# Kernel optimization log

Measured on AMD Instinct MI355X. Metric: run time of the kernel, lower is better.

## Reference

```python
import jax, jax.numpy as jnp
import numpy as np

NUM_CLASSES = 256
MARGIN = 0.3
EPS = 1e-12  # torch F.normalize eps


def setup_inputs() -> dict:
    key = jax.random.key(0)
    k1, k2 = jax.random.split(key)
    embeddings = jax.random.normal(k1, (65536, 512), dtype=jnp.float32)
    labels = jax.random.randint(k2, (65536,), 0, NUM_CLASSES)
    return {"embeddings": embeddings, "labels": labels}


def _l2_normalize(x):
    n = jnp.linalg.norm(x, axis=-1, keepdims=True)
    return x / jnp.maximum(n, EPS)


def reference(embeddings, labels):
    # emb_norm: (B, d)
    emb = _l2_normalize(embeddings)

    # Per-class segment mean -> centroids (C, d)
    counts = jax.ops.segment_sum(jnp.ones((emb.shape[0],), emb.dtype), labels,
                                 num_segments=NUM_CLASSES)          # (C,)
    sums = jax.ops.segment_sum(emb, labels, num_segments=NUM_CLASSES)  # (C, d)
    present = counts > 0                                              # (C,)
    cent = sums / jnp.maximum(counts, 1.0)[:, None]
    cent = _l2_normalize(cent)

    # Pairwise centroid euclidean distances (centroids are unit-norm).
    # Only used for argmin (no grad path), so stop_gradient for safety.
    cg = jax.lax.stop_gradient(cent)
    dist = jnp.sqrt(jnp.clip(2.0 - 2.0 * (cg @ cg.T), 0.0))           # (C, C)
    inf = jnp.asarray(jnp.inf, dist.dtype)
    dist = jnp.where(jnp.eye(NUM_CLASSES, dtype=bool), inf, dist)
    dist = jnp.where(present[None, :], dist, inf)  # empty classes can't be negatives
    nearest = jnp.argmin(dist, axis=1)                                # (C,)

    # Gather positive / nearest-negative centroid per sample
    pos_c = cent[labels]                 # (B, d)
    neg_c = cent[nearest[labels]]        # (B, d)
    d_pos = 1.0 - jnp.sum(emb * pos_c, axis=1)
    d_neg = 1.0 - jnp.sum(emb * neg_c, axis=1)
    terms = jax.nn.relu(d_pos - d_neg + MARGIN)                       # (B,)

    # Per-class mean of triplet terms, then mean over present classes
    loss_c = jax.ops.segment_sum(terms, labels, num_segments=NUM_CLASSES)
    loss_c = loss_c / jnp.maximum(counts, 1.0)
    n_present = jnp.maximum(jnp.sum(present.astype(emb.dtype)), 1.0)
    loss = jnp.sum(jnp.where(present, loss_c, 0.0)) / n_present
    return loss
```

## Files before the change

### kernel.cpp

```cpp
#include <hip/hip_runtime.h>
#include <math.h>

#define BROWS 65536
#define DIMS 512
#define NCLS 256
#define MARGIN 0.3f
#define EPSN 1e-12f
#define TSPL 8
#define CURPAD 16

__global__ void __launch_bounds__(256) khist(const int* __restrict__ labels,
                                             float* __restrict__ counts) {
  __shared__ int h[NCLS];
  int t = threadIdx.x;
  h[t] = 0;
  __syncthreads();
  int base = blockIdx.x * 2048 + t;
#pragma unroll
  for (int k = 0; k < 8; ++k) atomicAdd(&h[labels[base + k * 256]], 1);
  __syncthreads();
  if (h[t] > 0) unsafeAtomicAdd(&counts[t], (float)h[t]);
}

__global__ void __launch_bounds__(256) kbase(const float* __restrict__ counts,
                                             int* __restrict__ bases,
                                             int* __restrict__ cursor) {
  int t = threadIdx.x;
  __shared__ int sc[NCLS];
  sc[t] = (int)counts[t];
  __syncthreads();
  int v = sc[t];
  for (int off = 1; off < NCLS; off <<= 1) {
    int add = (t >= off) ? sc[t - off] : 0;
    __syncthreads();
    sc[t] = v = v + add;
    __syncthreads();
  }
  int excl = (t == 0) ? 0 : sc[t - 1];
  bases[t] = excl;
  cursor[t * CURPAD] = excl;
}

__global__ void __launch_bounds__(256) kscatter(const int* __restrict__ labels,
                                                int* __restrict__ cursor,
                                                int* __restrict__ rowidx) {
  int r = blockIdx.x * blockDim.x + threadIdx.x;
  int lab = labels[r];
  int pos = atomicAdd(&cursor[lab * CURPAD], 1);
  rowidx[pos] = r;
}

__global__ void __launch_bounds__(256) ksumn(const float* __restrict__ emb,
                                             const int* __restrict__ rowidx,
                                             const int* __restrict__ bases,
                                             const float* __restrict__ counts,
                                             float* __restrict__ invnorm,
                                             float* __restrict__ partials,
                                             int lsplits) {
  int splits = 1 << lsplits;
  int cls = blockIdx.x >> lsplits;
  int sp = blockIdx.x & (splits - 1);
  int t = threadIdx.x, w = t >> 6, lane = t & 63;
  int base = bases[cls];
  int cnt = (int)counts[cls];
  int i0 = (cnt * sp) >> lsplits;
  int i1 = (cnt * (sp + 1)) >> lsplits;
  int n = i1 - i0;
  int j0 = i0 + ((n * w) >> 2);
  int j1 = i0 + ((n * (w + 1)) >> 2);
  const float4* ebase = reinterpret_cast<const float4*>(emb);
  int cq = lane * 2;
  float4 acc0 = make_float4(0.f, 0.f, 0.f, 0.f);
  float4 acc1 = make_float4(0.f, 0.f, 0.f, 0.f);
  int j = j0;
  for (; j + 4 <= j1; j += 4) {
    int r[4];
#pragma unroll
    for (int k = 0; k < 4; ++k) r[k] = rowidx[base + j + k];
    float4 a[4], b[4];
#pragma unroll
    for (int k = 0; k < 4; ++k) {
      const float4* p = ebase + (size_t)r[k] * (DIMS / 4) + cq;
      a[k] = p[0];
      b[k] = p[1];
    }
    float s[4];
#pragma unroll
    for (int k = 0; k < 4; ++k)
      s[k] = a[k].x*a[k].x + a[k].y*a[k].y + a[k].z*a[k].z + a[k].w*a[k].w
           + b[k].x*b[k].x + b[k].y*b[k].y + b[k].z*b[k].z + b[k].w*b[k].w;
#pragma unroll
    for (int off = 1; off < 64; off <<= 1) {
#pragma unroll
      for (int k = 0; k < 4; ++k) s[k] += __shfl_xor(s[k], off, 64);
    }
    float q[4];
#pragma unroll
    for (int k = 0; k < 4; ++k) q[k] = 1.0f / fmaxf(sqrtf(s[k]), EPSN);
    if (lane == 0) {
      invnorm[r[0]] = q[0]; invnorm[r[1]] = q[1];
      invnorm[r[2]] = q[2]; invnorm[r[3]] = q[3];
    }
#pragma unroll
    for (int k = 0; k < 4; ++k) {
      acc0.x += a[k].x * q[k]; acc0.y += a[k].y * q[k];
      acc0.z += a[k].z * q[k]; acc0.w += a[k].w * q[k];
      acc1.x += b[k].x * q[k]; acc1.y += b[k].y * q[k];
      acc1.z += b[k].z * q[k]; acc1.w += b[k].w * q[k];
    }
  }
  for (; j < j1; ++j) {
    int r0 = rowidx[base + j];
    const float4* p = ebase + (size_t)r0 * (DIMS / 4) + cq;
    float4 a = p[0], b = p[1];
    float s = a.x*a.x + a.y*a.y + a.z*a.z + a.w*a.w
            + b.x*b.x + b.y*b.y + b.z*b.z + b.w*b.w;
#pragma unroll
    for (int off = 1; off < 64; off <<= 1) s += __shfl_xor(s, off, 64);
    float q0 = 1.0f / fmaxf(sqrtf(s), EPSN);
    if (lane == 0) invnorm[r0] = q0;
    acc0.x += a.x * q0; acc0.y += a.y * q0; acc0.z += a.z * q0; acc0.w += a.w * q0;
    acc1.x += b.x * q0; acc1.y += b.y * q0; acc1.z += b.z * q0; acc1.w += b.w * q0;
  }
  __shared__ float lds[4][DIMS];
  *reinterpret_cast<float4*>(&lds[w][lane * 8]) = acc0;
  *reinterpret_cast<float4*>(&lds[w][lane * 8 + 4]) = acc1;
  __syncthreads();
  float o0 = lds[0][t] + lds[1][t] + lds[2][t] + lds[3][t];
  float o1 = lds[0][t + 256] + lds[1][t + 256] + lds[2][t + 256] + lds[3][t + 256];
  float* outp = partials + ((size_t)sp * NCLS + cls) * DIMS;
  outp[t] = o0;
  outp[t + 256] = o1;
}

__global__ void __launch_bounds__(256) kcent(const float* __restrict__ partials,
                                             const float* __restrict__ counts,
                                             float* __restrict__ cent, int splits) {
  int cls = blockIdx.x, t = threadIdx.x;
  float s0 = 0.0f, s1 = 0.0f;
  for (int sp = 0; sp < splits; ++sp) {
    const float* p = partials + ((size_t)sp * NCLS + cls) * DIMS;
    s0 += p[t];
    s1 += p[t + 256];
  }
  float cm = fmaxf(counts[cls], 1.0f);
  float m0 = s0 / cm, m1 = s1 / cm;
  __shared__ float red[256];
  red[t] = m0 * m0 + m1 * m1;
  __syncthreads();
  for (int off = 128; off > 0; off >>= 1) {
    if (t < off) red[t] += red[t + off];
    __syncthreads();
  }
  float inv = 1.0f / fmaxf(sqrtf(red[0]), EPSN);
  cent[(size_t)cls * DIMS + t] = m0 * inv;
  cent[(size_t)cls * DIMS + t + 256] = m1 * inv;
}

__global__ void __launch_bounds__(256) knearest(const float* __restrict__ cent,
                                                const float* __restrict__ counts,
                                                int* __restrict__ nearest) {
  int i = blockIdx.x, j = threadIdx.x;
  __shared__ float ci[DIMS];
  ci[j] = cent[(size_t)i * DIMS + j];
  ci[j + 256] = cent[(size_t)i * DIMS + j + 256];
  __syncthreads();
  const float4* cj = reinterpret_cast<const float4*>(cent + (size_t)j * DIMS);
  float dot = 0.0f;
#pragma unroll 8
  for (int k = 0; k < DIMS / 4; ++k) {
    float4 v = cj[k];
    dot += v.x * ci[4*k] + v.y * ci[4*k+1] + v.z * ci[4*k+2] + v.w * ci[4*k+3];
  }
  float dist = sqrtf(fmaxf(2.0f - 2.0f * dot, 0.0f));
  bool valid = (j != i) && (counts[j] > 0.0f);
  float dv = valid ? dist : INFINITY;
  __shared__ float sd[256];
  __shared__ int si[256];
  sd[j] = dv; si[j] = j;
  __syncthreads();
  for (int off = 128; off > 0; off >>= 1) {
    if (j < off) {
      float o = sd[j + off]; int oi = si[j + off];
      if (o < sd[j] || (o == sd[j] && oi < si[j])) { sd[j] = o; si[j] = oi; }
    }
    __syncthreads();
  }
  if (j == 0) nearest[i] = si[0];
}

__global__ void __launch_bounds__(256) kterm2(const float* __restrict__ emb,
                                              const float* __restrict__ invnorm,
                                              const int* __restrict__ rowidx,
                                              const int* __restrict__ bases,
                                              const float* __restrict__ counts,
                                              const float* __restrict__ cent,
                                              const int* __restrict__ nearest,
                                              float* __restrict__ tsums) {
  int cls = blockIdx.x >> 3;
  int sp = blockIdx.x & (TSPL - 1);
  int t = threadIdx.x, w = t >> 6, lane = t & 63;
  int base = bases[cls];
  int cnt = (int)counts[cls];
  int ng = nearest[cls];
  int cq = lane * 2;
  const float4* pp = reinterpret_cast<const float4*>(cent + (size_t)cls * DIMS) + cq;
  const float4* pn = reinterpret_cast<const float4*>(cent + (size_t)ng * DIMS) + cq;
  float4 P0 = pp[0], P1 = pp[1], N0 = pn[0], N1 = pn[1];
  float4 d0 = make_float4(N0.x - P0.x, N0.y - P0.y, N0.z - P0.z, N0.w - P0.w);
  float4 d1 = make_float4(N1.x - P1.x, N1.y - P1.y, N1.z - P1.z, N1.w - P1.w);
  int i0 = (cnt * sp) / TSPL;
  int i1 = (cnt * (sp + 1)) / TSPL;
  int n = i1 - i0;
  int j0 = i0 + ((n * w) >> 2);
  int j1 = i0 + ((n * (w + 1)) >> 2);
  const float4* ebase = reinterpret_cast<const float4*>(emb);
  float tsum = 0.0f;
  int j = j0;
  for (; j + 4 <= j1; j += 4) {
    int r[4];
#pragma unroll
    for (int k = 0; k < 4; ++k) r[k] = rowidx[base + j + k];
    float4 a[4], b[4];
#pragma unroll
    for (int k = 0; k < 4; ++k) {
      const float4* p = ebase + (size_t)r[k] * (DIMS / 4) + cq;
      a[k] = p[0];
      b[k] = p[1];
    }
    float s[4];
#pragma unroll
    for (int k = 0; k < 4; ++k)
      s[k] = a[k].x*d0.x + a[k].y*d0.y + a[k].z*d0.z + a[k].w*d0.w
           + b[k].x*d1.x + b[k].y*d1.y + b[k].z*d1.z + b[k].w*d1.w;
#pragma unroll
    for (int off = 1; off < 64; off <<= 1) {
#pragma unroll
      for (int k = 0; k < 4; ++k) s[k] += __shfl_xor(s[k], off, 64);
    }
#pragma unroll
    for (int k = 0; k < 4; ++k)
      tsum += fmaxf(s[k] * invnorm[r[k]] + MARGIN, 0.0f);
  }
  for (; j < j1; ++j) {
    int r0 = rowidx[base + j];
    const float4* p = ebase + (size_t)r0 * (DIMS / 4) + cq;
    float4 a = p[0], b = p[1];
    float s = a.x*d0.x + a.y*d0.y + a.z*d0.z + a.w*d0.w
            + b.x*d1.x + b.y*d1.y + b.z*d1.z + b.w*d1.w;
#pragma unroll
    for (int off = 1; off < 64; off <<= 1) s += __shfl_xor(s, off, 64);
    tsum += fmaxf(s * invnorm[r0] + MARGIN, 0.0f);
  }
  __shared__ float sred[4];
  if (lane == 0) sred[w] = tsum;
  __syncthreads();
  if (t == 0) tsums[blockIdx.x] = sred[0] + sred[1] + sred[2] + sred[3];
}

__global__ void __launch_bounds__(256) kfinal(const float* __restrict__ counts,
                                              const float* __restrict__ tsums,
                                              float* __restrict__ out) {
  int t = threadIdx.x;
  float cnt = counts[t];
  bool present = cnt > 0.0f;
  float ls = 0.0f;
#pragma unroll
  for (int k = 0; k < TSPL; ++k) ls += tsums[t * TSPL + k];
  float v = present ? ls / fmaxf(cnt, 1.0f) : 0.0f;
  float np = present ? 1.0f : 0.0f;
  __shared__ float sv[256], sp[256];
  sv[t] = v; sp[t] = np;
  __syncthreads();
  for (int off = 128; off > 0; off >>= 1) {
    if (t < off) { sv[t] += sv[t + off]; sp[t] += sp[t + off]; }
    __syncthreads();
  }
  if (t == 0) out[0] = sv[0] / fmaxf(sp[0], 1.0f);
}

extern "C" void kernel_launch(void* const* d_in, const int* in_sizes, int n_in,
                              void* d_out, int out_size, void* d_ws, size_t ws_size,
                              hipStream_t stream) {
  const float* emb = (const float*)d_in[0];
  const int* labels = (const int*)d_in[1];
  float* out = (float*)d_out;

  char* ws = (char*)d_ws;
  size_t off = 0;
  auto alloc = [&](size_t bytes) {
    char* p = ws + off;
    off += (bytes + 255) & ~(size_t)255;
    return p;
  };
  float* invnorm = (float*)alloc((size_t)BROWS * 4);
  float* counts  = (float*)alloc((size_t)NCLS * 4);
  float* cent    = (float*)alloc((size_t)NCLS * DIMS * 4);
  int*   nearest = (int*)alloc((size_t)NCLS * 4);
  int*   bases   = (int*)alloc((size_t)NCLS * 4);
  int*   cursor  = (int*)alloc((size_t)NCLS * CURPAD * 4);
  int*   rowidx  = (int*)alloc((size_t)BROWS * 4);
  float* tsums   = (float*)alloc((size_t)NCLS * TSPL * 4);
  size_t fixed = off;

  int lsplits = 3;
  while (lsplits > 0 &&
         fixed + (((size_t)NCLS * DIMS * 4) << lsplits) > ws_size) lsplits--;
  int splits = 1 << lsplits;
  float* partials = (float*)alloc(((size_t)NCLS * DIMS * 4) << lsplits);

  hipMemsetAsync(counts, 0, NCLS * sizeof(float), stream);

  khist<<<32, 256, 0, stream>>>(labels, counts);
  kbase<<<1, 256, 0, stream>>>(counts, bases, cursor);
  kscatter<<<BROWS / 256, 256, 0, stream>>>(labels, cursor, rowidx);
  ksumn<<<NCLS * splits, 256, 0, stream>>>(emb, rowidx, bases, counts,
                                           invnorm, partials, lsplits);
  kcent<<<NCLS, 256, 0, stream>>>(partials, counts, cent, splits);
  knearest<<<NCLS, 256, 0, stream>>>(cent, counts, nearest);
  kterm2<<<NCLS * TSPL, 256, 0, stream>>>(emb, invnorm, rowidx, bases, counts,
                                          cent, nearest, tsums);
  kfinal<<<1, 256, 0, stream>>>(counts, tsums, out);
}
```

Baseline: 258.4 us.

## Store normalized embeddings as bf16 for second pass and restructure class bucketing

The first pass now writes each normalized embedding row as packed bf16 into a workspace buffer. The second pass reads that half-size copy instead of re-reading fp32 embeddings and per-row inverse norms, and its unroll goes from 4 to 8 rows. The counting and bucketing is replaced by a per-strip histogram plus a scatter that uses local offsets, which removes the memset, the global atomics and one kernel launch. Extra write traffic in the first pass and bf16 rounding error in the triplet dot products are the costs, and the fixed workspace size is no longer checked against ws_size.

Result: faster. 253.0 us (-2.1%).

```diff
diff --git a/kernel.cpp b/kernel.cpp
--- a/kernel.cpp
+++ b/kernel.cpp
@@ -6,28 +6,47 @@
 #define NCLS 256
 #define MARGIN 0.3f
 #define EPSN 1e-12f
+#define NSTRIP 64
+#define SROWS 1024
+#define LSPL 3
 #define TSPL 8
-#define CURPAD 16
-
-__global__ void __launch_bounds__(256) khist(const int* __restrict__ labels,
-                                             float* __restrict__ counts) {
+
+__device__ __forceinline__ unsigned pk2(float lo, float hi) {
+  unsigned a = __float_as_uint(lo), b = __float_as_uint(hi);
+  a = (a + 0x7FFFu + ((a >> 16) & 1u)) >> 16;
+  b = (b + 0x7FFFu + ((b >> 16) & 1u)) & 0xFFFF0000u;
+  return a | b;
+}
+__device__ __forceinline__ float uplo(unsigned u) { return __uint_as_float(u << 16); }
+__device__ __forceinline__ float uphi(unsigned u) { return __uint_as_float(u & 0xFFFF0000u); }
+
+__global__ void __launch_bounds__(256) khist2(const int* __restrict__ labels,
+                                              int* __restrict__ hist) {
   __shared__ int h[NCLS];
-  int t = threadIdx.x;
+  int t = threadIdx.x, s = blockIdx.x;
   h[t] = 0;
   __syncthreads();
-  int base = blockIdx.x * 2048 + t;
-#pragma unroll
-  for (int k = 0; k < 8; ++k) atomicAdd(&h[labels[base + k * 256]], 1);
-  __syncthreads();
-  if (h[t] > 0) unsafeAtomicAdd(&counts[t], (float)h[t]);
-}
-
-__global__ void __launch_bounds__(256) kbase(const float* __restrict__ counts,
-                                             int* __restrict__ bases,
-                                             int* __restrict__ cursor) {
-  int t = threadIdx.x;
+  int base = s * SROWS + t;
+#pragma unroll
+  for (int k = 0; k < SROWS / 256; ++k) atomicAdd(&h[labels[base + k * 256]], 1);
+  __syncthreads();
+  hist[s * NCLS + t] = h[t];
+}
+
+__global__ void __launch_bounds__(256) kscatter2(const int* __restrict__ labels,
+                                                 const int* __restrict__ hist,
+                                                 int* __restrict__ bases,
+                                                 float* __restrict__ counts,
+                                                 int* __restrict__ rowidx) {
+  int t = threadIdx.x, s = blockIdx.x;
+  int run = 0, myoff = 0;
+  for (int s2 = 0; s2 < NSTRIP; ++s2) {
+    int h = hist[s2 * NCLS + t];
+    if (s2 < s) myoff += h;
+    run += h;
+  }
   __shared__ int sc[NCLS];
-  sc[t] = (int)counts[t];
+  sc[t] = run;
   __syncthreads();
   int v = sc[t];
   for (int off = 1; off < NCLS; off <<= 1) {
@@ -37,34 +56,38 @@
     __syncthreads();
   }
   int excl = (t == 0) ? 0 : sc[t - 1];
-  bases[t] = excl;
-  cursor[t * CURPAD] = excl;
-}
-
-__global__ void __launch_bounds__(256) kscatter(const int* __restrict__ labels,
-                                                int* __restrict__ cursor,
-                                                int* __restrict__ rowidx) {
-  int r = blockIdx.x * blockDim.x + threadIdx.x;
-  int lab = labels[r];
-  int pos = atomicAdd(&cursor[lab * CURPAD], 1);
-  rowidx[pos] = r;
+  if (s == 0) {
+    bases[t] = excl;
+    counts[t] = (float)run;
+  }
+  __shared__ int loff[NCLS];
+  __shared__ int cur[NCLS];
+  loff[t] = excl + myoff;
+  cur[t] = 0;
+  __syncthreads();
+  int rbase = s * SROWS + t;
+#pragma unroll
+  for (int k = 0; k < SROWS / 256; ++k) {
+    int r = rbase + k * 256;
+    int lab = labels[r];
+    int lpos = atomicAdd(&cur[lab], 1);
+    rowidx[loff[lab] + lpos] = r;
+  }
 }
 
 __global__ void __launch_bounds__(256) ksumn(const float* __restrict__ emb,
                                              const int* __restrict__ rowidx,
                                              const int* __restrict__ bases,
                                              const float* __restrict__ counts,
-                                             float* __restrict__ invnorm,
-                                             float* __restrict__ partials,
-                                             int lsplits) {
-  int splits = 1 << lsplits;
-  int cls = blockIdx.x >> lsplits;
-  int sp = blockIdx.x & (splits - 1);
+                                             uint4* __restrict__ embn,
+                                             float* __restrict__ partials) {
+  int cls = blockIdx.x >> LSPL;
+  int sp = blockIdx.x & ((1 << LSPL) - 1);
   int t = threadIdx.x, w = t >> 6, lane = t & 63;
   int base = bases[cls];
   int cnt = (int)counts[cls];
-  int i0 = (cnt * sp) >> lsplits;
-  int i1 = (cnt * (sp + 1)) >> lsplits;
+  int i0 = (cnt * sp) >> LSPL;
+  int i1 = (cnt * (sp + 1)) >> LSPL;
   int n = i1 - i0;
   int j0 = i0 + ((n * w) >> 2);
   int j1 = i0 + ((n * (w + 1)) >> 2);
@@ -97,16 +120,18 @@
     float q[4];
 #pragma unroll
     for (int k = 0; k < 4; ++k) q[k] = 1.0f / fmaxf(sqrtf(s[k]), EPSN);
-    if (lane == 0) {
-      invnorm[r[0]] = q[0]; invnorm[r[1]] = q[1];
-      invnorm[r[2]] = q[2]; invnorm[r[3]] = q[3];
-    }
 #pragma unroll
     for (int k = 0; k < 4; ++k) {
-      acc0.x += a[k].x * q[k]; acc0.y += a[k].y * q[k];
-      acc0.z += a[k].z * q[k]; acc0.w += a[k].w * q[k];
-      acc1.x += b[k].x * q[k]; acc1.y += b[k].y * q[k];
-      acc1.z += b[k].z * q[k]; acc1.w += b[k].w * q[k];
+      float nx0 = a[k].x * q[k], ny0 = a[k].y * q[k];
+      float nz0 = a[k].z * q[k], nw0 = a[k].w * q[k];
+      float nx1 = b[k].x * q[k], ny1 = b[k].y * q[k];
+      float nz1 = b[k].z * q[k], nw1 = b[k].w * q[k];
+      acc0.x += nx0; acc0.y += ny0; acc0.z += nz0; acc0.w += nw0;
+      acc1.x += nx1; acc1.y += ny1; acc1.z += nz1; acc1.w += nw1;
+      uint4 o;
+      o.x = pk2(nx0, ny0); o.y = pk2(nz0, nw0);
+      o.z = pk2(nx1, ny1); o.w = pk2(nz1, nw1);
+      embn[(size_t)r[k] * (DIMS / 8) + lane] = o;
     }
   }
   for (; j < j1; ++j) {
@@ -118,9 +143,14 @@
 #pragma unroll
     for (int off = 1; off < 64; off <<= 1) s += __shfl_xor(s, off, 64);
     float q0 = 1.0f / fmaxf(sqrtf(s), EPSN);
-    if (lane == 0) invnorm[r0] = q0;
-    acc0.x += a.x * q0; acc0.y += a.y * q0; acc0.z += a.z * q0; acc0.w += a.w * q0;
-    acc1.x += b.x * q0; acc1.y += b.y * q0; acc1.z += b.z * q0; acc1.w += b.w * q0;
+    float nx0 = a.x*q0, ny0 = a.y*q0, nz0 = a.z*q0, nw0 = a.w*q0;
+    float nx1 = b.x*q0, ny1 = b.y*q0, nz1 = b.z*q0, nw1 = b.w*q0;
+    acc0.x += nx0; acc0.y += ny0; acc0.z += nz0; acc0.w += nw0;
+    acc1.x += nx1; acc1.y += ny1; acc1.z += nz1; acc1.w += nw1;
+    uint4 o;
+    o.x = pk2(nx0, ny0); o.y = pk2(nz0, nw0);
+    o.z = pk2(nx1, ny1); o.w = pk2(nz1, nw1);
+    embn[(size_t)r0 * (DIMS / 8) + lane] = o;
   }
   __shared__ float lds[4][DIMS];
   *reinterpret_cast<float4*>(&lds[w][lane * 8]) = acc0;
@@ -135,10 +165,11 @@
 
 __global__ void __launch_bounds__(256) kcent(const float* __restrict__ partials,
                                              const float* __restrict__ counts,
-                                             float* __restrict__ cent, int splits) {
+                                             float* __restrict__ cent) {
   int cls = blockIdx.x, t = threadIdx.x;
   float s0 = 0.0f, s1 = 0.0f;
-  for (int sp = 0; sp < splits; ++sp) {
+#pragma unroll
+  for (int sp = 0; sp < (1 << LSPL); ++sp) {
     const float* p = partials + ((size_t)sp * NCLS + cls) * DIMS;
     s0 += p[t];
     s1 += p[t + 256];
@@ -189,8 +220,7 @@
   if (j == 0) nearest[i] = si[0];
 }
 
-__global__ void __launch_bounds__(256) kterm2(const float* __restrict__ emb,
-                                              const float* __restrict__ invnorm,
+__global__ void __launch_bounds__(256) kterm2(const uint4* __restrict__ embn,
                                               const int* __restrict__ rowidx,
                                               const int* __restrict__ bases,
                                               const float* __restrict__ counts,
@@ -214,43 +244,36 @@
   int n = i1 - i0;
   int j0 = i0 + ((n * w) >> 2);
   int j1 = i0 + ((n * (w + 1)) >> 2);
-  const float4* ebase = reinterpret_cast<const float4*>(emb);
   float tsum = 0.0f;
   int j = j0;
-  for (; j + 4 <= j1; j += 4) {
-    int r[4];
-#pragma unroll
-    for (int k = 0; k < 4; ++k) r[k] = rowidx[base + j + k];
-    float4 a[4], b[4];
-#pragma unroll
-    for (int k = 0; k < 4; ++k) {
-      const float4* p = ebase + (size_t)r[k] * (DIMS / 4) + cq;
-      a[k] = p[0];
-      b[k] = p[1];
-    }
-    float s[4];
-#pragma unroll
-    for (int k = 0; k < 4; ++k)
-      s[k] = a[k].x*d0.x + a[k].y*d0.y + a[k].z*d0.z + a[k].w*d0.w
-           + b[k].x*d1.x + b[k].y*d1.y + b[k].z*d1.z + b[k].w*d1.w;
+  for (; j + 8 <= j1; j += 8) {
+    int r[8];
+#pragma unroll
+    for (int k = 0; k < 8; ++k) r[k] = rowidx[base + j + k];
+    uint4 v[8];
+#pragma unroll
+    for (int k = 0; k < 8; ++k) v[k] = embn[(size_t)r[k] * (DIMS / 8) + lane];
+    float s[8];
+#pragma unroll
+    for (int k = 0; k < 8; ++k)
+      s[k] = uplo(v[k].x)*d0.x + uphi(v[k].x)*d0.y + uplo(v[k].y)*d0.z + uphi(v[k].y)*d0.w
+           + uplo(v[k].z)*d1.x + uphi(v[k].z)*d1.y + uplo(v[k].w)*d1.z + uphi(v[k].w)*d1.w;
 #pragma unroll
     for (int off = 1; off < 64; off <<= 1) {
 #pragma unroll
-      for (int k = 0; k < 4; ++k) s[k] += __shfl_xor(s[k], off, 64);
-    }
-#pragma unroll
-    for (int k = 0; k < 4; ++k)
-      tsum += fmaxf(s[k] * invnorm[r[k]] + MARGIN, 0.0f);
+      for (int k = 0; k < 8; ++k) s[k] += __shfl_xor(s[k], off, 64);
+    }
+#pragma unroll
+    for (int k = 0; k < 8; ++k) tsum += fmaxf(s[k] + MARGIN, 0.0f);
   }
   for (; j < j1; ++j) {
     int r0 = rowidx[base + j];
-    const float4* p = ebase + (size_t)r0 * (DIMS / 4) + cq;
-    float4 a = p[0], b = p[1];
-    float s = a.x*d0.x + a.y*d0.y + a.z*d0.z + a.w*d0.w
-            + b.x*d1.x + b.y*d1.y + b.z*d1.z + b.w*d1.w;
+    uint4 v = embn[(size_t)r0 * (DIMS / 8) + lane];
+    float s = uplo(v.x)*d0.x + uphi(v.x)*d0.y + uplo(v.y)*d0.z + uphi(v.y)*d0.w
+            + uplo(v.z)*d1.x + uphi(v.z)*d1.y + uplo(v.w)*d1.z + uphi(v.w)*d1.w;
 #pragma unroll
     for (int off = 1; off < 64; off <<= 1) s += __shfl_xor(s, off, 64);
-    tsum += fmaxf(s * invnorm[r0] + MARGIN, 0.0f);
+    tsum += fmaxf(s + MARGIN, 0.0f);
   }
   __shared__ float sred[4];
   if (lane == 0) sred[w] = tsum;
@@ -293,32 +316,21 @@
     off += (bytes + 255) & ~(size_t)255;
     return p;
   };
-  float* invnorm = (float*)alloc((size_t)BROWS * 4);
+  int*   hist    = (int*)alloc((size_t)NSTRIP * NCLS * 4);
+  int*   bases   = (int*)alloc((size_t)NCLS * 4);
   float* counts  = (float*)alloc((size_t)NCLS * 4);
   float* cent    = (float*)alloc((size_t)NCLS * DIMS * 4);
   int*   nearest = (int*)alloc((size_t)NCLS * 4);
-  int*   bases   = (int*)alloc((size_t)NCLS * 4);
-  int*   cursor  = (int*)alloc((size_t)NCLS * CURPAD * 4);
   int*   rowidx  = (int*)alloc((size_t)BROWS * 4);
   float* tsums   = (float*)alloc((size_t)NCLS * TSPL * 4);
-  size_t fixed = off;
-
-  int lsplits = 3;
-  while (lsplits > 0 &&
-         fixed + (((size_t)NCLS * DIMS * 4) << lsplits) > ws_size) lsplits--;
-  int splits = 1 << lsplits;
-  float* partials = (float*)alloc(((size_t)NCLS * DIMS * 4) << lsplits);
-
-  hipMemsetAsync(counts, 0, NCLS * sizeof(float), stream);
-
-  khist<<<32, 256, 0, stream>>>(labels, counts);
-  kbase<<<1, 256, 0, stream>>>(counts, bases, cursor);
-  kscatter<<<BROWS / 256, 256, 0, stream>>>(labels, cursor, rowidx);
-  ksumn<<<NCLS * splits, 256, 0, stream>>>(emb, rowidx, bases, counts,
-                                           invnorm, partials, lsplits);
-  kcent<<<NCLS, 256, 0, stream>>>(partials, counts, cent, splits);
+  float* partials= (float*)alloc(((size_t)NCLS * DIMS * 4) << LSPL);
+  uint4* embn    = (uint4*)alloc((size_t)BROWS * DIMS * 2);
+
+  khist2<<<NSTRIP, 256, 0, stream>>>(labels, hist);
+  kscatter2<<<NSTRIP, 256, 0, stream>>>(labels, hist, bases, counts, rowidx);
+  ksumn<<<NCLS << LSPL, 256, 0, stream>>>(emb, rowidx, bases, counts, embn, partials);
+  kcent<<<NCLS, 256, 0, stream>>>(partials, counts, cent);
   knearest<<<NCLS, 256, 0, stream>>>(cent, counts, nearest);
-  kterm2<<<NCLS * TSPL, 256, 0, stream>>>(emb, invnorm, rowidx, bases, counts,
-                                          cent, nearest, tsums);
+  kterm2<<<NCLS * TSPL, 256, 0, stream>>>(embn, rowidx, bases, counts, cent, nearest, tsums);
   kfinal<<<1, 256, 0, stream>>>(counts, tsums, out);
 }
```
